# Kernel tuning notes

Measured on AMD Instinct MI355X. Metric: run time of the kernel, lower is better.

The kernel has to match this reference:

```python
import jax, jax.numpy as jnp
import numpy as np

SLACKNESS_PENALTY = 1.0
WEIGHT_DECAY = 1e-5

POS_LEN, NUM_NEG = 32768, 64
N_RULES, N_UNLABEL = 262144, 131072
NUM_ENT, NUM_REL, EMB_DIM = 100000, 500, 256


def _rand_triples(key, n):
    k1, k2, k3 = jax.random.split(key, 3)
    h = jax.random.randint(k1, (n,), 0, NUM_ENT)
    r = jax.random.randint(k2, (n,), 0, NUM_REL)
    t = jax.random.randint(k3, (n,), 0, NUM_ENT)
    return jnp.stack([h, r, t], axis=1)  # [n, 3]


def setup_inputs() -> dict:
    key = jax.random.key(0)
    ks = jax.random.split(key, 10)
    pos_score = jax.random.normal(ks[0], (POS_LEN, 1), dtype=jnp.float32)
    neg_score = jax.random.normal(ks[1], (POS_LEN, NUM_NEG), dtype=jnp.float32)
    confidence = jax.random.uniform(ks[2], (N_RULES,), dtype=jnp.float32)
    ent_emb = jax.random.normal(ks[3], (NUM_ENT, EMB_DIM), dtype=jnp.float32) * 0.1
    rel_emb = jax.random.normal(ks[4], (NUM_REL, EMB_DIM), dtype=jnp.float32) * 0.1
    rule_p1 = _rand_triples(ks[5], N_RULES)
    rule_p2 = _rand_triples(ks[6], N_RULES)
    triple_num = jax.random.randint(ks[7], (N_RULES,), 2, 4)  # values in {2, 3}
    unlabel_ids = jax.random.randint(ks[8], (N_RULES,), 0, N_UNLABEL)
    unlabel_triples = _rand_triples(ks[9], N_UNLABEL)
    return dict(pos_score=pos_score, neg_score=neg_score, confidence=confidence,
                ent_emb=ent_emb, rel_emb=rel_emb, rule_p1=rule_p1, rule_p2=rule_p2,
                triple_num=triple_num, unlabel_ids=unlabel_ids,
                unlabel_triples=unlabel_triples)


def _score(triples, ent_emb, rel_emb):
    # DistMult KGE score: sum_d e_h * w_r * e_t  -> [n, 1]
    h = ent_emb[triples[:, 0]]
    r = rel_emb[triples[:, 1]]
    t = ent_emb[triples[:, 2]]
    return jnp.sum(h * r * t, axis=-1, keepdims=True)


def reference(pos_score, neg_score, confidence, ent_emb, rel_emb,
              rule_p1, rule_p2, triple_num, unlabel_ids, unlabel_triples):
    # BCE(sigmoid(pos), 1) = softplus(-x); BCE(sigmoid(neg), 0) = softplus(x)
    positive_loss = jnp.mean(jax.nn.softplus(-pos_score))
    negative_loss = jnp.mean(jax.nn.softplus(neg_score))

    # Per-rule body sigmoids (originally memoized one-row model() calls)
    s1 = jax.nn.sigmoid(_score(rule_p1, ent_emb, rel_emb))[:, 0]  # [n_rules]
    s2 = jax.nn.sigmoid(_score(rule_p2, ent_emb, rel_emb))[:, 0]
    contrib = SLACKNESS_PENALTY * confidence * s1 * jnp.where(triple_num == 3, s2, 1.0)
    # pi_gradient dict scatter-add -> segment_sum over unique unlabel triples
    pi_grad = jax.ops.segment_sum(contrib, unlabel_ids,
                                  num_segments=unlabel_triples.shape[0])  # [n_unlabel]

    su = _score(unlabel_triples, ent_emb, rel_emb)  # [n_unlabel, 1]
    p = jax.nn.sigmoid(su)
    # target = clip(p + pi_grad, 0, 1), detached (original uses .cpu().detach().numpy())
    tgt = jax.lax.stop_gradient(jnp.clip(p + pi_grad[:, None], 0.0, 1.0))
    # BCE(p, tgt) with stable log-sigmoid forms
    unlabel_loss = jnp.mean(tgt * jax.nn.softplus(-su) + (1.0 - tgt) * jax.nn.softplus(su))

    regularization = WEIGHT_DECAY * (jnp.sum(ent_emb ** 2) + jnp.sum(rel_emb ** 2))
    return positive_loss + negative_loss + unlabel_loss + regularization
```

## Files before the change

kernel.cpp:

```cpp
#include <hip/hip_runtime.h>
#include <cstddef>
#include <cstdint>

#define POS_LEN    32768
#define NUM_NEG    64
#define N_RULES    262144
#define N_UNLABEL  131072
#define NUM_ENT    100000
#define NUM_REL    500
#define EMB_DIM    256
#define WEIGHT_DECAY 1e-5

#define AUX_BLOCKS    2048
#define GATHER_BLOCKS 2048
#define LOSS_BLOCKS   1024

typedef __attribute__((ext_vector_type(4))) float        f32x4;
typedef __attribute__((ext_vector_type(2))) unsigned int u32x2;
typedef __attribute__((ext_vector_type(4))) unsigned int u32x4;

__device__ __forceinline__ float softplusf_(float x) {
    return fmaxf(x, 0.0f) + log1pf(expf(-fabsf(x)));
}
__device__ __forceinline__ float sigmoidf_(float x) {
    return 1.0f / (1.0f + expf(-x));
}
__device__ __forceinline__ float quarter_sum16(float v) {
#pragma unroll
    for (int m = 1; m <= 8; m <<= 1) v += __shfl_xor(v, m, 64);
    return v;
}
__device__ __forceinline__ float wave_sum64(float v) {
#pragma unroll
    for (int m = 32; m >= 1; m >>= 1) v += __shfl_xor(v, m, 64);
    return v;
}
__device__ __forceinline__ double wave_sum64d(double v) {
#pragma unroll
    for (int m = 32; m >= 1; m >>= 1) v += __shfl_xor(v, m, 64);
    return v;
}

__device__ __forceinline__ u32x2 f32x8_to_fp8(const f32x4 a, const f32x4 b) {
    int lo = 0, hi = 0;
    lo = __builtin_amdgcn_cvt_pk_fp8_f32(a[0], a[1], lo, false);
    lo = __builtin_amdgcn_cvt_pk_fp8_f32(a[2], a[3], lo, true);
    hi = __builtin_amdgcn_cvt_pk_fp8_f32(b[0], b[1], hi, false);
    hi = __builtin_amdgcn_cvt_pk_fp8_f32(b[2], b[3], hi, true);
    u32x2 r; r[0] = (unsigned)lo; r[1] = (unsigned)hi; return r;
}
__device__ __forceinline__ void fp8x4_to_f32(unsigned int w, float* o) {
    auto x = __builtin_amdgcn_cvt_pk_f32_fp8((int)w, false);
    auto y = __builtin_amdgcn_cvt_pk_f32_fp8((int)w, true);
    o[0] = x[0]; o[1] = x[1]; o[2] = y[0]; o[3] = y[1];
}

__device__ __forceinline__ float dot3_q(const u32x4 hv, const u32x4 rv, const u32x4 tv) {
    float s = 0.0f;
#pragma unroll
    for (int w = 0; w < 4; ++w) {
        float hf[4], rf[4], tf[4];
        fp8x4_to_f32(hv[w], hf);
        fp8x4_to_f32(rv[w], rf);
        fp8x4_to_f32(tv[w], tf);
        s = fmaf(hf[0] * rf[0], tf[0], s);
        s = fmaf(hf[1] * rf[1], tf[1], s);
        s = fmaf(hf[2] * rf[2], tf[2], s);
        s = fmaf(hf[3] * rf[3], tf[3], s);
    }
    return quarter_sum16(s);
}

__global__ void aux_fp8_kernel(const float* __restrict__ ent,
                               const float* __restrict__ rel,
                               u32x2* __restrict__ ent8,
                               u32x2* __restrict__ rel8,
                               float* __restrict__ pi_grad,
                               float* __restrict__ auxp) {
    const int tid = blockIdx.x * blockDim.x + threadIdx.x;
    const int stride = gridDim.x * blockDim.x;
    for (int i = tid; i < N_UNLABEL; i += stride) pi_grad[i] = 0.0f;
    float sq = 0.0f;
    const f32x4* entv = reinterpret_cast<const f32x4*>(ent);
    for (int i = tid; i < (NUM_ENT * EMB_DIM) / 8; i += stride) {
        f32x4 a = __builtin_nontemporal_load(entv + (size_t)i * 2);
        f32x4 b = __builtin_nontemporal_load(entv + (size_t)i * 2 + 1);
        sq += a[0]*a[0] + a[1]*a[1] + a[2]*a[2] + a[3]*a[3]
            + b[0]*b[0] + b[1]*b[1] + b[2]*b[2] + b[3]*b[3];
        ent8[i] = f32x8_to_fp8(a, b);
    }
    const f32x4* relv = reinterpret_cast<const f32x4*>(rel);
    for (int i = tid; i < (NUM_REL * EMB_DIM) / 8; i += stride) {
        f32x4 a = __builtin_nontemporal_load(relv + (size_t)i * 2);
        f32x4 b = __builtin_nontemporal_load(relv + (size_t)i * 2 + 1);
        sq += a[0]*a[0] + a[1]*a[1] + a[2]*a[2] + a[3]*a[3]
            + b[0]*b[0] + b[1]*b[1] + b[2]*b[2] + b[3]*b[3];
        rel8[i] = f32x8_to_fp8(a, b);
    }
    sq = wave_sum64(sq);
    __shared__ float ls[8];
    const int lane = threadIdx.x & 63, wid = threadIdx.x >> 6;
    if (lane == 0) ls[wid] = sq;
    __syncthreads();
    if (threadIdx.x == 0) {
        float bs = 0.0f;
        for (int w = 0; w < (int)(blockDim.x >> 6); ++w) bs += ls[w];
        auxp[blockIdx.x] = bs;
    }
}

__global__ void gather_kernel(const float* __restrict__ conf,
                              const u32x4* __restrict__ ent8,
                              const u32x4* __restrict__ rel8,
                              const int* __restrict__ p1,
                              const int* __restrict__ p2,
                              const int* __restrict__ tnum,
                              const int* __restrict__ uids,
                              const int* __restrict__ ut,
                              float* __restrict__ pi_grad,
                              float* __restrict__ su_out) {
    const int lane = threadIdx.x & 63;
    const int l    = lane & 15;
    const int q    = lane >> 4;
    const int wave  = blockIdx.x * (blockDim.x >> 6) + (threadIdx.x >> 6);
    const int nwave = gridDim.x * (blockDim.x >> 6);
    const int nr4 = N_RULES / 4, nu4 = N_UNLABEL / 4, ntot = nr4 + nu4;

    for (int pi = wave; pi < ntot; pi += nwave) {
        if (pi < nr4) {
            const int rule = pi * 4 + q;
            const int b = rule * 3;
            const int h1 = p1[b], r1 = p1[b + 1], t1 = p1[b + 2];
            const int tn = tnum[rule];
            const float cf = conf[rule];
            const int uid = uids[rule];
            const bool has2 = (tn == 3);
            const u32x4 H1 = ent8[(size_t)h1 * 16 + l];
            const u32x4 R1 = rel8[(size_t)r1 * 16 + l];
            const u32x4 T1 = ent8[(size_t)t1 * 16 + l];
            u32x4 H2 = {0, 0, 0, 0}, R2 = {0, 0, 0, 0}, T2 = {0, 0, 0, 0};
            if (has2) {
                const int h2 = p2[b], r2 = p2[b + 1], t2 = p2[b + 2];
                H2 = ent8[(size_t)h2 * 16 + l];
                R2 = rel8[(size_t)r2 * 16 + l];
                T2 = ent8[(size_t)t2 * 16 + l];
            }
            float c = sigmoidf_(dot3_q(H1, R1, T1)) * cf;
            if (has2) c *= sigmoidf_(dot3_q(H2, R2, T2));
            if (l == 0) atomicAdd(&pi_grad[uid], c);
        } else {
            const int i = (pi - nr4) * 4 + q;
            const int b = i * 3;
            const int h = ut[b], r = ut[b + 1], t = ut[b + 2];
            const u32x4 H = ent8[(size_t)h * 16 + l];
            const u32x4 R = rel8[(size_t)r * 16 + l];
            const u32x4 T = ent8[(size_t)t * 16 + l];
            const float su = dot3_q(H, R, T);
            if (l == 0) su_out[i] = su;
        }
    }
}

__global__ void loss_kernel(const float* __restrict__ su,
                            const float* __restrict__ pi_grad,
                            const float* __restrict__ pos,
                            const float* __restrict__ neg,
                            float* __restrict__ lossp) {
    const int tid = blockIdx.x * blockDim.x + threadIdx.x;
    const int stride = gridDim.x * blockDim.x;
    float ul = 0.0f, ps = 0.0f, ns = 0.0f;
    for (int i = tid; i < N_UNLABEL; i += stride) {
        const float s   = su[i];
        const float p   = sigmoidf_(s);
        const float tgt = fminf(fmaxf(p + pi_grad[i], 0.0f), 1.0f);
        ul += tgt * softplusf_(-s) + (1.0f - tgt) * softplusf_(s);
    }
    const f32x4* posv = reinterpret_cast<const f32x4*>(pos);
    for (int i = tid; i < POS_LEN / 4; i += stride) {
        f32x4 v = __builtin_nontemporal_load(posv + i);
        ps += softplusf_(-v[0]) + softplusf_(-v[1]) + softplusf_(-v[2]) + softplusf_(-v[3]);
    }
    const f32x4* negv = reinterpret_cast<const f32x4*>(neg);
    for (int i = tid; i < (POS_LEN * NUM_NEG) / 4; i += stride) {
        f32x4 v = __builtin_nontemporal_load(negv + i);
        ns += softplusf_(v[0]) + softplusf_(v[1]) + softplusf_(v[2]) + softplusf_(v[3]);
    }
    ul = wave_sum64(ul); ps = wave_sum64(ps); ns = wave_sum64(ns);
    __shared__ float lu[8], lp[8], ln[8];
    const int lane = threadIdx.x & 63, wid = threadIdx.x >> 6;
    if (lane == 0) { lu[wid] = ul; lp[wid] = ps; ln[wid] = ns; }
    __syncthreads();
    if (threadIdx.x == 0) {
        float bu = 0.0f, bp = 0.0f, bn = 0.0f;
        for (int w = 0; w < (int)(blockDim.x >> 6); ++w) { bu += lu[w]; bp += lp[w]; bn += ln[w]; }
        lossp[blockIdx.x]                   = bu;
        lossp[LOSS_BLOCKS + blockIdx.x]     = bp;
        lossp[2 * LOSS_BLOCKS + blockIdx.x] = bn;
    }
}

__global__ void finalize_kernel(const float* __restrict__ auxp,
                                const float* __restrict__ lossp,
                                float* __restrict__ out) {
    const int lane = threadIdx.x;
    double sq = 0.0, ul = 0.0, ps = 0.0, ns = 0.0;
    for (int i = lane; i < AUX_BLOCKS; i += 64) sq += (double)auxp[i];
    for (int i = lane; i < LOSS_BLOCKS; i += 64) {
        ul += (double)lossp[i];
        ps += (double)lossp[LOSS_BLOCKS + i];
        ns += (double)lossp[2 * LOSS_BLOCKS + i];
    }
    sq = wave_sum64d(sq); ul = wave_sum64d(ul);
    ps = wave_sum64d(ps); ns = wave_sum64d(ns);
    if (lane == 0) {
        double v = ps / (double)POS_LEN
                 + ns / ((double)POS_LEN * (double)NUM_NEG)
                 + ul / (double)N_UNLABEL
                 + WEIGHT_DECAY * sq;
        out[0] = (float)v;
    }
}

extern "C" void kernel_launch(void* const* d_in, const int* in_sizes, int n_in,
                              void* d_out, int out_size, void* d_ws, size_t ws_size,
                              hipStream_t stream) {
    const float* pos  = (const float*)d_in[0];
    const float* neg  = (const float*)d_in[1];
    const float* conf = (const float*)d_in[2];
    const float* ent  = (const float*)d_in[3];
    const float* rel  = (const float*)d_in[4];
    const int*   p1   = (const int*)d_in[5];
    const int*   p2   = (const int*)d_in[6];
    const int*   tnum = (const int*)d_in[7];
    const int*   uids = (const int*)d_in[8];
    const int*   ut   = (const int*)d_in[9];

    const size_t off_pi    = 0;
    const size_t off_su    = off_pi + (size_t)N_UNLABEL * 4;
    const size_t off_auxp  = off_su + (size_t)N_UNLABEL * 4;
    const size_t off_lossp = off_auxp + (size_t)AUX_BLOCKS * 4;
    const size_t off_tab   = (off_lossp + (size_t)3 * LOSS_BLOCKS * 4 + 511) & ~(size_t)511;
    const size_t off_rel8  = off_tab + (size_t)NUM_ENT * EMB_DIM;

    float* pi_grad = (float*)((char*)d_ws + off_pi);
    float* su      = (float*)((char*)d_ws + off_su);
    float* auxp    = (float*)((char*)d_ws + off_auxp);
    float* lossp   = (float*)((char*)d_ws + off_lossp);
    u32x2* ent8w   = (u32x2*)((char*)d_ws + off_tab);
    u32x2* rel8w   = (u32x2*)((char*)d_ws + off_rel8);

    aux_fp8_kernel<<<AUX_BLOCKS, 256, 0, stream>>>(ent, rel, ent8w, rel8w, pi_grad, auxp);
    gather_kernel<<<GATHER_BLOCKS, 256, 0, stream>>>(conf,
                                                     (const u32x4*)((char*)d_ws + off_tab),
                                                     (const u32x4*)((char*)d_ws + off_rel8),
                                                     p1, p2, tnum, uids, ut, pi_grad, su);
    loss_kernel<<<LOSS_BLOCKS, 256, 0, stream>>>(su, pi_grad, pos, neg, lossp);
    finalize_kernel<<<1, 64, 0, stream>>>(auxp, lossp, (float*)d_out);
}
```

Baseline: 101.3 us.

## Software-pipeline gather index loads and widen fp8 conversion stores

The gather kernel drops the unified grid-stride loop over rules and unlabeled triples. Rules now run in a fixed-count loop that prefetches the next rule's indices, confidence and uid while the current embedding rows load. Unlabeled triples run in a separate loop that processes two per iteration to give more loads in flight, and the index loads use nontemporal hints. The fp8 conversion kernel now handles 16 floats per thread and writes 16-byte stores. Launch bounds are added to all three kernels. The fixed iteration counts assume the sizes divide evenly and that the grid size matches the compile-time wave count, which the launch satisfies.

Measured after the change: 115.2 us. +13.7%, slower.

```diff
diff --git a/kernel.cpp b/kernel.cpp
--- a/kernel.cpp
+++ b/kernel.cpp
@@ -14,6 +14,10 @@
 #define AUX_BLOCKS    2048
 #define GATHER_BLOCKS 2048
 #define LOSS_BLOCKS   1024
+
+#define NWAVE   (GATHER_BLOCKS * 4)
+#define R_ITERS (N_RULES / 4 / NWAVE)
+#define U_ITERS (N_UNLABEL / 4 / NWAVE)
 
 typedef __attribute__((ext_vector_type(4))) float        f32x4;
 typedef __attribute__((ext_vector_type(2))) unsigned int u32x2;
@@ -71,31 +75,46 @@
     return quarter_sum16(s);
 }
 
-__global__ void aux_fp8_kernel(const float* __restrict__ ent,
-                               const float* __restrict__ rel,
-                               u32x2* __restrict__ ent8,
-                               u32x2* __restrict__ rel8,
-                               float* __restrict__ pi_grad,
-                               float* __restrict__ auxp) {
+__global__ __launch_bounds__(256) void aux_fp8_kernel(const float* __restrict__ ent,
+                                                      const float* __restrict__ rel,
+                                                      u32x4* __restrict__ ent8,
+                                                      u32x4* __restrict__ rel8,
+                                                      float* __restrict__ pi_grad,
+                                                      float* __restrict__ auxp) {
     const int tid = blockIdx.x * blockDim.x + threadIdx.x;
     const int stride = gridDim.x * blockDim.x;
     for (int i = tid; i < N_UNLABEL; i += stride) pi_grad[i] = 0.0f;
+
     float sq = 0.0f;
     const f32x4* entv = reinterpret_cast<const f32x4*>(ent);
-    for (int i = tid; i < (NUM_ENT * EMB_DIM) / 8; i += stride) {
-        f32x4 a = __builtin_nontemporal_load(entv + (size_t)i * 2);
-        f32x4 b = __builtin_nontemporal_load(entv + (size_t)i * 2 + 1);
+    for (int i = tid; i < (NUM_ENT * EMB_DIM) / 16; i += stride) {
+        f32x4 a = __builtin_nontemporal_load(entv + (size_t)i * 4);
+        f32x4 b = __builtin_nontemporal_load(entv + (size_t)i * 4 + 1);
+        f32x4 c = __builtin_nontemporal_load(entv + (size_t)i * 4 + 2);
+        f32x4 d = __builtin_nontemporal_load(entv + (size_t)i * 4 + 3);
         sq += a[0]*a[0] + a[1]*a[1] + a[2]*a[2] + a[3]*a[3]
-            + b[0]*b[0] + b[1]*b[1] + b[2]*b[2] + b[3]*b[3];
-        ent8[i] = f32x8_to_fp8(a, b);
+            + b[0]*b[0] + b[1]*b[1] + b[2]*b[2] + b[3]*b[3]
+            + c[0]*c[0] + c[1]*c[1] + c[2]*c[2] + c[3]*c[3]
+            + d[0]*d[0] + d[1]*d[1] + d[2]*d[2] + d[3]*d[3];
+        u32x2 lo = f32x8_to_fp8(a, b);
+        u32x2 hi = f32x8_to_fp8(c, d);
+        u32x4 o; o[0] = lo[0]; o[1] = lo[1]; o[2] = hi[0]; o[3] = hi[1];
+        ent8[i] = o;
     }
     const f32x4* relv = reinterpret_cast<const f32x4*>(rel);
-    for (int i = tid; i < (NUM_REL * EMB_DIM) / 8; i += stride) {
-        f32x4 a = __builtin_nontemporal_load(relv + (size_t)i * 2);
-        f32x4 b = __builtin_nontemporal_load(relv + (size_t)i * 2 + 1);
+    for (int i = tid; i < (NUM_REL * EMB_DIM) / 16; i += stride) {
+        f32x4 a = __builtin_nontemporal_load(relv + (size_t)i * 4);
+        f32x4 b = __builtin_nontemporal_load(relv + (size_t)i * 4 + 1);
+        f32x4 c = __builtin_nontemporal_load(relv + (size_t)i * 4 + 2);
+        f32x4 d = __builtin_nontemporal_load(relv + (size_t)i * 4 + 3);
         sq += a[0]*a[0] + a[1]*a[1] + a[2]*a[2] + a[3]*a[3]
-            + b[0]*b[0] + b[1]*b[1] + b[2]*b[2] + b[3]*b[3];
-        rel8[i] = f32x8_to_fp8(a, b);
+            + b[0]*b[0] + b[1]*b[1] + b[2]*b[2] + b[3]*b[3]
+            + c[0]*c[0] + c[1]*c[1] + c[2]*c[2] + c[3]*c[3]
+            + d[0]*d[0] + d[1]*d[1] + d[2]*d[2] + d[3]*d[3];
+        u32x2 lo = f32x8_to_fp8(a, b);
+        u32x2 hi = f32x8_to_fp8(c, d);
+        u32x4 o; o[0] = lo[0]; o[1] = lo[1]; o[2] = hi[0]; o[3] = hi[1];
+        rel8[i] = o;
     }
     sq = wave_sum64(sq);
     __shared__ float ls[8];
@@ -109,63 +128,95 @@
     }
 }
 
-__global__ void gather_kernel(const float* __restrict__ conf,
-                              const u32x4* __restrict__ ent8,
-                              const u32x4* __restrict__ rel8,
-                              const int* __restrict__ p1,
-                              const int* __restrict__ p2,
-                              const int* __restrict__ tnum,
-                              const int* __restrict__ uids,
-                              const int* __restrict__ ut,
-                              float* __restrict__ pi_grad,
-                              float* __restrict__ su_out) {
+__global__ __launch_bounds__(256, 8) void gather_kernel(const float* __restrict__ conf,
+                                                        const u32x4* __restrict__ ent8,
+                                                        const u32x4* __restrict__ rel8,
+                                                        const int* __restrict__ p1,
+                                                        const int* __restrict__ p2,
+                                                        const int* __restrict__ tnum,
+                                                        const int* __restrict__ uids,
+                                                        const int* __restrict__ ut,
+                                                        float* __restrict__ pi_grad,
+                                                        float* __restrict__ su_out) {
     const int lane = threadIdx.x & 63;
     const int l    = lane & 15;
     const int q    = lane >> 4;
-    const int wave  = blockIdx.x * (blockDim.x >> 6) + (threadIdx.x >> 6);
-    const int nwave = gridDim.x * (blockDim.x >> 6);
-    const int nr4 = N_RULES / 4, nu4 = N_UNLABEL / 4, ntot = nr4 + nu4;
-
-    for (int pi = wave; pi < ntot; pi += nwave) {
-        if (pi < nr4) {
-            const int rule = pi * 4 + q;
-            const int b = rule * 3;
-            const int h1 = p1[b], r1 = p1[b + 1], t1 = p1[b + 2];
-            const int tn = tnum[rule];
-            const float cf = conf[rule];
-            const int uid = uids[rule];
-            const bool has2 = (tn == 3);
-            const u32x4 H1 = ent8[(size_t)h1 * 16 + l];
-            const u32x4 R1 = rel8[(size_t)r1 * 16 + l];
-            const u32x4 T1 = ent8[(size_t)t1 * 16 + l];
-            u32x4 H2 = {0, 0, 0, 0}, R2 = {0, 0, 0, 0}, T2 = {0, 0, 0, 0};
-            if (has2) {
-                const int h2 = p2[b], r2 = p2[b + 1], t2 = p2[b + 2];
-                H2 = ent8[(size_t)h2 * 16 + l];
-                R2 = rel8[(size_t)r2 * 16 + l];
-                T2 = ent8[(size_t)t2 * 16 + l];
+    const int wave = blockIdx.x * 4 + (threadIdx.x >> 6);
+
+    int rule = wave * 4 + q;
+    int h1 = __builtin_nontemporal_load(p1 + rule * 3);
+    int r1 = __builtin_nontemporal_load(p1 + rule * 3 + 1);
+    int t1 = __builtin_nontemporal_load(p1 + rule * 3 + 2);
+    int tn = __builtin_nontemporal_load(tnum + rule);
+    float cf = __builtin_nontemporal_load(conf + rule);
+    int uid = __builtin_nontemporal_load(uids + rule);
+    int h2 = 0, r2 = 0, t2 = 0;
+    if (tn == 3) {
+        h2 = __builtin_nontemporal_load(p2 + rule * 3);
+        r2 = __builtin_nontemporal_load(p2 + rule * 3 + 1);
+        t2 = __builtin_nontemporal_load(p2 + rule * 3 + 2);
+    }
+    for (int k = 0; k < R_ITERS; ++k) {
+        const bool  has2  = (tn == 3);
+        const float cf_c  = cf;
+        const int   uid_c = uid;
+        const u32x4 H1 = ent8[(size_t)h1 * 16 + l];
+        const u32x4 R1 = rel8[(size_t)r1 * 16 + l];
+        const u32x4 T1 = ent8[(size_t)t1 * 16 + l];
+        u32x4 H2v = {0,0,0,0}, R2v = {0,0,0,0}, T2v = {0,0,0,0};
+        if (has2) {
+            H2v = ent8[(size_t)h2 * 16 + l];
+            R2v = rel8[(size_t)r2 * 16 + l];
+            T2v = ent8[(size_t)t2 * 16 + l];
+        }
+        if (k + 1 < R_ITERS) {
+            rule += NWAVE * 4;
+            h1 = __builtin_nontemporal_load(p1 + rule * 3);
+            r1 = __builtin_nontemporal_load(p1 + rule * 3 + 1);
+            t1 = __builtin_nontemporal_load(p1 + rule * 3 + 2);
+            tn = __builtin_nontemporal_load(tnum + rule);
+            cf = __builtin_nontemporal_load(conf + rule);
+            uid = __builtin_nontemporal_load(uids + rule);
+            if (tn == 3) {
+                h2 = __builtin_nontemporal_load(p2 + rule * 3);
+                r2 = __builtin_nontemporal_load(p2 + rule * 3 + 1);
+                t2 = __builtin_nontemporal_load(p2 + rule * 3 + 2);
             }
-            float c = sigmoidf_(dot3_q(H1, R1, T1)) * cf;
-            if (has2) c *= sigmoidf_(dot3_q(H2, R2, T2));
-            if (l == 0) atomicAdd(&pi_grad[uid], c);
-        } else {
-            const int i = (pi - nr4) * 4 + q;
-            const int b = i * 3;
-            const int h = ut[b], r = ut[b + 1], t = ut[b + 2];
-            const u32x4 H = ent8[(size_t)h * 16 + l];
-            const u32x4 R = rel8[(size_t)r * 16 + l];
-            const u32x4 T = ent8[(size_t)t * 16 + l];
-            const float su = dot3_q(H, R, T);
-            if (l == 0) su_out[i] = su;
         }
-    }
-}
-
-__global__ void loss_kernel(const float* __restrict__ su,
-                            const float* __restrict__ pi_grad,
-                            const float* __restrict__ pos,
-                            const float* __restrict__ neg,
-                            float* __restrict__ lossp) {
+        float c = sigmoidf_(dot3_q(H1, R1, T1)) * cf_c;
+        if (has2) c *= sigmoidf_(dot3_q(H2v, R2v, T2v));
+        if (l == 0) atomicAdd(&pi_grad[uid_c], c);
+    }
+
+    for (int k = 0; k < U_ITERS; k += 2) {
+        const int i0 = (wave + k * NWAVE) * 4 + q;
+        const int i1 = i0 + NWAVE * 4;
+        const int ha = __builtin_nontemporal_load(ut + i0 * 3);
+        const int ra = __builtin_nontemporal_load(ut + i0 * 3 + 1);
+        const int ta = __builtin_nontemporal_load(ut + i0 * 3 + 2);
+        const int hb = __builtin_nontemporal_load(ut + i1 * 3);
+        const int rb = __builtin_nontemporal_load(ut + i1 * 3 + 1);
+        const int tb = __builtin_nontemporal_load(ut + i1 * 3 + 2);
+        const u32x4 HA = ent8[(size_t)ha * 16 + l];
+        const u32x4 RA = rel8[(size_t)ra * 16 + l];
+        const u32x4 TA = ent8[(size_t)ta * 16 + l];
+        const u32x4 HB = ent8[(size_t)hb * 16 + l];
+        const u32x4 RB = rel8[(size_t)rb * 16 + l];
+        const u32x4 TB = ent8[(size_t)tb * 16 + l];
+        const float sa = dot3_q(HA, RA, TA);
+        const float sb = dot3_q(HB, RB, TB);
+        if (l == 0) {
+            su_out[i0] = sa;
+            su_out[i1] = sb;
+        }
+    }
+}
+
+__global__ __launch_bounds__(256) void loss_kernel(const float* __restrict__ su,
+                                                   const float* __restrict__ pi_grad,
+                                                   const float* __restrict__ pos,
+                                                   const float* __restrict__ neg,
+                                                   float* __restrict__ lossp) {
     const int tid = blockIdx.x * blockDim.x + threadIdx.x;
     const int stride = gridDim.x * blockDim.x;
     float ul = 0.0f, ps = 0.0f, ns = 0.0f;
@@ -246,13 +297,11 @@
     float* su      = (float*)((char*)d_ws + off_su);
     float* auxp    = (float*)((char*)d_ws + off_auxp);
     float* lossp   = (float*)((char*)d_ws + off_lossp);
-    u32x2* ent8w   = (u32x2*)((char*)d_ws + off_tab);
-    u32x2* rel8w   = (u32x2*)((char*)d_ws + off_rel8);
-
-    aux_fp8_kernel<<<AUX_BLOCKS, 256, 0, stream>>>(ent, rel, ent8w, rel8w, pi_grad, auxp);
-    gather_kernel<<<GATHER_BLOCKS, 256, 0, stream>>>(conf,
-                                                     (const u32x4*)((char*)d_ws + off_tab),
-                                                     (const u32x4*)((char*)d_ws + off_rel8),
+    u32x4* ent8    = (u32x4*)((char*)d_ws + off_tab);
+    u32x4* rel8    = (u32x4*)((char*)d_ws + off_rel8);
+
+    aux_fp8_kernel<<<AUX_BLOCKS, 256, 0, stream>>>(ent, rel, ent8, rel8, pi_grad, auxp);
+    gather_kernel<<<GATHER_BLOCKS, 256, 0, stream>>>(conf, ent8, rel8,
                                                      p1, p2, tnum, uids, ut, pi_grad, su);
     loss_kernel<<<LOSS_BLOCKS, 256, 0, stream>>>(su, pi_grad, pos, neg, lossp);
     finalize_kernel<<<1, 64, 0, stream>>>(auxp, lossp, (float*)d_out);
```
